# Kernel tuning notes

Measured on AMD Instinct MI355X. Metric: run time of the kernel, lower is better.

The kernel has to match this reference:

```python
import jax, jax.numpy as jnp
import numpy as np

# Physical constants hardcoded in the torch module: m=[1.0, 50.0], l=[1.0, 1.0], g=10.0
M_DIAG = jnp.array([1.0, 1.0, 50.0, 50.0], dtype=jnp.float32)  # mass matrix diagonal [m0,m0,m1,m1]
G = 10.0


def _phi(x):
    # x: [4] = (x0, y0, x1, y1); two holonomic rod-length constraints
    c1 = x[0] ** 2 + x[1] ** 2 - 1.0
    c2 = (x[0] - x[2]) ** 2 + (x[1] - x[3]) ** 2 - 1.0
    return jnp.stack([c1, c2])  # [2]


def _potential(x):
    # U = sum_i m_i * g * y_i  (y coords are x[1], x[3])
    return M_DIAG[0] * G * x[1] + M_DIAG[2] * G * x[3]


def _forward(coords):
    x, v = jnp.split(coords, 2, axis=-1)  # each [bs, 4]
    minv = (1.0 / M_DIAG).astype(coords.dtype)  # diagonal of M^{-1}, [4]

    # phi_q[:, i] = d phi_i / dx  -> [bs, 2, 4]
    phi_q = jax.vmap(jax.jacfwd(_phi))(x)

    # phi_qq[:, i] = d/dx ( phi_q[i] . v )  -> [bs, 2, 4]
    def _gdot(xi, vi):
        return jax.jacfwd(_phi)(xi) @ vi  # [2]

    phi_qq = jax.vmap(jax.jacfwd(_gdot, argnums=0))(x, v)

    # F = -dV/dx  -> [bs, 4]
    F = -jax.vmap(jax.grad(_potential))(x)

    # Minv is diagonal: phi_q @ Minv == phi_q * minv (broadcast over last axis)
    phiq_Minv = phi_q * minv  # [bs, 2, 4]

    L = jnp.einsum('bik,bjk->bij', phiq_Minv, phi_q)  # [bs, 2, 2]
    R = jnp.einsum('bik,bk->bi', phiq_Minv, F) + jnp.einsum('bik,bk->bi', phi_qq, v)  # [bs, 2]
    lam = jnp.einsum('bij,bj->bi', jnp.linalg.inv(L), R)  # [bs, 2]

    a = minv * (F - jnp.einsum('bik,bi->bk', phi_q, lam))  # [bs, 4]
    return jnp.concatenate([v, a], axis=-1)  # [bs, 8]


def setup_inputs() -> dict:
    key = jax.random.key(0)
    coords = jax.random.normal(key, (2097152, 8), dtype=jnp.float32)
    t = jnp.zeros((1,), dtype=jnp.float32)
    return {"t": t, "coords": coords}


def reference(t, coords):
    # t is unused in the dynamics (autonomous system), matching the torch forward
    return _forward(coords)
```

## Files before the change

### kernel.cpp

```cpp
#include <hip/hip_runtime.h>


typedef float vfloat4_t __attribute__((ext_vector_type(4)));

#define UNROLL 8

__device__ __forceinline__ float4 pend2_process(float4 mine, bool odd) {
    float4 other;
    other.x = __shfl_xor(mine.x, 1);
    other.y = __shfl_xor(mine.y, 1);
    other.z = __shfl_xor(mine.z, 1);
    other.w = __shfl_xor(mine.w, 1);

    float4 p = odd ? other : mine;
    float4 q = odd ? mine : other;

    float x0 = p.x, y0 = p.y, x1 = p.z, y1 = p.w;
    float u0 = q.x, w0 = q.y, u1 = q.z, w1 = q.w;

    float dx = x0 - x1, dy = y0 - y1;
    float du = u0 - u1, dw = w0 - w1;

    float L11 = 4.0f * (x0 * x0 + y0 * y0);
    float L12 = 4.0f * (x0 * dx + y0 * dy);
    float L22 = 4.08f * (dx * dx + dy * dy);

    float R1 = -20.0f * y0 + 2.0f * (u0 * u0 + w0 * w0);
    float R2 = 2.0f * (du * du + dw * dw);

    float det = L11 * L22 - L12 * L12;
    float inv = 1.0f / det;
    float lam1 = (L22 * R1 - L12 * R2) * inv;
    float lam2 = (L11 * R2 - L12 * R1) * inv;

    float4 res;
    if (odd) {
        res.x = -2.0f * (x0 * lam1 + dx * lam2);
        res.y = -10.0f - 2.0f * (y0 * lam1 + dy * lam2);
        res.z = 0.04f * dx * lam2;
        res.w = -10.0f + 0.04f * dy * lam2;
    } else {
        res = q;
    }
    return res;
}

__global__ __launch_bounds__(256) void pend2_dae_kernel(
    const float4* __restrict__ in,
    float4* __restrict__ out,
    int n4)
{
    const int NT  = gridDim.x * blockDim.x;
    const int t   = blockIdx.x * blockDim.x + threadIdx.x;
    const bool odd = (t & 1);

    const int span  = NT * UNROLL;
    const int nfull = (n4 / span) * span;

    for (int base = 0; base < nfull; base += span) {
        float4 v[UNROLL];
        #pragma unroll
        for (int k = 0; k < UNROLL; ++k)
            v[k] = in[base + k * NT + t];

        #pragma unroll
        for (int k = 0; k < UNROLL; ++k) {
            float4 r = pend2_process(v[k], odd);
            out[base + k * NT + t] = r;
        }
    }

    for (int j = nfull + t; j < n4; j += NT) {
        float4 r = pend2_process(in[j], odd);
        out[j] = r;
    }
}

extern "C" void kernel_launch(void* const* d_in, const int* in_sizes, int n_in,
                              void* d_out, int out_size, void* d_ws, size_t ws_size,
                              hipStream_t stream) {
    const float4* coords = (const float4*)d_in[1];
    float4* out = (float4*)d_out;
    int n4 = in_sizes[1] / 4;

    int block = 256;
    long long want = ((long long)n4 + (long long)block * UNROLL - 1)
                     / ((long long)block * UNROLL);
    int grid = (int)(want < 1 ? 1 : (want > 2048 ? 2048 : want));
    pend2_dae_kernel<<<grid, block, 0, stream>>>(coords, out, n4);
}
```

Baseline: 118.7 us.

## Use one thread per element with DPP lane swap and nontemporal stores

Replaces the grid-stride unrolled loop with a simple one-thread-per-float4 launch that covers the whole array. The cross-lane exchange moves from __shfl_xor, which goes through LDS permute, to a DPP quad-permute move that stays in registers. Output is written with nontemporal stores so the streamed result does not pollute cache. The trade-off is many more blocks and less memory-level parallelism per thread than the unrolled loads gave.

```diff
diff --git a/kernel.cpp b/kernel.cpp
--- a/kernel.cpp
+++ b/kernel.cpp
@@ -3,15 +3,29 @@
 
 typedef float vfloat4_t __attribute__((ext_vector_type(4)));
 
-#define UNROLL 8
+__device__ __forceinline__ float dpp_swap1(float x) {
+    int i = __builtin_bit_cast(int, x);
+    i = __builtin_amdgcn_mov_dpp(i, 0xB1, 0xF, 0xF, true);
+    return __builtin_bit_cast(float, i);
+}
 
-__device__ __forceinline__ float4 pend2_process(float4 mine, bool odd) {
+__global__ __launch_bounds__(256) void pend2_dae_kernel(
+    const float4* __restrict__ in,
+    float4* __restrict__ out,
+    int n4)
+{
+    int j = blockIdx.x * blockDim.x + threadIdx.x;
+    if (j >= n4) return;
+
+    float4 mine = in[j];
+
     float4 other;
-    other.x = __shfl_xor(mine.x, 1);
-    other.y = __shfl_xor(mine.y, 1);
-    other.z = __shfl_xor(mine.z, 1);
-    other.w = __shfl_xor(mine.w, 1);
+    other.x = dpp_swap1(mine.x);
+    other.y = dpp_swap1(mine.y);
+    other.z = dpp_swap1(mine.z);
+    other.w = dpp_swap1(mine.w);
 
+    bool odd = (j & 1);
     float4 p = odd ? other : mine;
     float4 q = odd ? mine : other;
 
@@ -33,47 +47,17 @@
     float lam1 = (L22 * R1 - L12 * R2) * inv;
     float lam2 = (L11 * R2 - L12 * R1) * inv;
 
-    float4 res;
+    vfloat4_t res;
     if (odd) {
         res.x = -2.0f * (x0 * lam1 + dx * lam2);
         res.y = -10.0f - 2.0f * (y0 * lam1 + dy * lam2);
         res.z = 0.04f * dx * lam2;
         res.w = -10.0f + 0.04f * dy * lam2;
     } else {
-        res = q;
-    }
-    return res;
-}
-
-__global__ __launch_bounds__(256) void pend2_dae_kernel(
-    const float4* __restrict__ in,
-    float4* __restrict__ out,
-    int n4)
-{
-    const int NT  = gridDim.x * blockDim.x;
-    const int t   = blockIdx.x * blockDim.x + threadIdx.x;
-    const bool odd = (t & 1);
-
-    const int span  = NT * UNROLL;
-    const int nfull = (n4 / span) * span;
-
-    for (int base = 0; base < nfull; base += span) {
-        float4 v[UNROLL];
-        #pragma unroll
-        for (int k = 0; k < UNROLL; ++k)
-            v[k] = in[base + k * NT + t];
-
-        #pragma unroll
-        for (int k = 0; k < UNROLL; ++k) {
-            float4 r = pend2_process(v[k], odd);
-            out[base + k * NT + t] = r;
-        }
+        res.x = q.x; res.y = q.y; res.z = q.z; res.w = q.w;
     }
 
-    for (int j = nfull + t; j < n4; j += NT) {
-        float4 r = pend2_process(in[j], odd);
-        out[j] = r;
-    }
+    __builtin_nontemporal_store(res, (vfloat4_t*)&out[j]);
 }
 
 extern "C" void kernel_launch(void* const* d_in, const int* in_sizes, int n_in,
@@ -84,8 +68,6 @@
     int n4 = in_sizes[1] / 4;
 
     int block = 256;
-    long long want = ((long long)n4 + (long long)block * UNROLL - 1)
-                     / ((long long)block * UNROLL);
-    int grid = (int)(want < 1 ? 1 : (want > 2048 ? 2048 : want));
+    int grid = (n4 + block - 1) / block;
     pend2_dae_kernel<<<grid, block, 0, stream>>>(coords, out, n4);
 }
```

Result: faster. 109.0 us (-8.2%).
